# Performance work log

Hardware: AMD Instinct MI355X
Metric: run time of the kernel (lower is better)

## Reference

```python
import jax, jax.numpy as jnp
import numpy as np
from jax import lax

NPOINT = 1024   # FPS centroids
NSAMPLE = 32    # neighbors per ball
RADIUS = 0.1    # ball-query radius (points live in unit cube)


def farthest_point_sample(pos, npoint):
    # pos: [B, N, 3] -> idx [B, npoint] int32
    B, N, _ = pos.shape

    def step(carry, _):
        min_d, far = carry                                   # [B,N], [B]
        centroid = jnp.take_along_axis(pos, far[:, None, None], axis=1)  # [B,1,3]
        d = jnp.sum((pos - centroid) ** 2, axis=-1)          # [B,N]
        min_d = jnp.minimum(min_d, d)
        nxt = jnp.argmax(min_d, axis=1).astype(jnp.int32)
        return (min_d, nxt), far

    init = (jnp.full((B, N), 1e10, pos.dtype), jnp.zeros((B,), jnp.int32))
    _, idx = lax.scan(step, init, None, length=npoint)
    return idx.T                                             # [B, npoint]


def ball_query(new_pos, pos, radius, k):
    # new_pos: [B,M,3], pos: [B,N,3] -> idx [B,M,k] int32
    d2 = (jnp.sum(new_pos ** 2, -1)[:, :, None]
          + jnp.sum(pos ** 2, -1)[:, None, :]
          - 2.0 * jnp.einsum('bmc,bnc->bmn', new_pos, pos))  # [B,M,N]
    neg = jnp.where(d2 <= radius * radius, -d2, -jnp.inf)
    vals, idx = lax.top_k(neg, k)                            # k nearest inside ball
    valid = vals > -jnp.inf
    idx = jnp.where(valid, idx, idx[..., :1])                # replicate first hit (centroid itself)
    return idx.astype(jnp.int32)


def setup_inputs() -> dict:
    key = jax.random.key(0)
    ks = jax.random.split(key, 6)
    B, N, C = 4, 16384, 1
    pos = jax.random.uniform(ks[0], (B, N, 3), dtype=jnp.float32)
    x = jax.random.normal(ks[1], (B, N, C), dtype=jnp.float32)
    c_in = 3 + C  # rel-xyz concat features
    W1 = jax.random.normal(ks[2], (c_in, 32), jnp.float32) * np.sqrt(2.0 / c_in)
    W2 = jax.random.normal(ks[3], (32, 32), jnp.float32) * np.sqrt(2.0 / 32)
    W3 = jax.random.normal(ks[4], (32, 32), jnp.float32) * np.sqrt(2.0 / 32)
    b1 = jnp.zeros((32,), jnp.float32)
    b2 = jnp.zeros((32,), jnp.float32)
    b3 = jnp.zeros((32,), jnp.float32)
    return {"pos": pos, "x": x, "W1": W1, "b1": b1, "W2": W2, "b2": b2, "W3": W3, "b3": b3}


def reference(pos, x, W1, b1, W2, b2, W3, b3):
    # PointNet++ set-abstraction: FPS -> ball query -> group -> shared MLP -> max-pool.
    fps_idx = farthest_point_sample(lax.stop_gradient(pos), NPOINT)       # [B,M]
    new_pos = jnp.take_along_axis(pos, fps_idx[..., None], axis=1)        # [B,M,3]
    idx = ball_query(lax.stop_gradient(new_pos), lax.stop_gradient(pos), RADIUS, NSAMPLE)  # [B,M,K]
    B, M, K = idx.shape
    flat = idx.reshape(B, M * K)
    gpos = jnp.take_along_axis(pos, flat[..., None], axis=1).reshape(B, M, K, 3)
    gx = jnp.take_along_axis(x, flat[..., None], axis=1).reshape(B, M, K, -1)
    rel = gpos - new_pos[:, :, None, :]                                   # local coords
    h = jnp.concatenate([rel, gx], axis=-1)                               # [B,M,K,4]
    h = jax.nn.relu(h @ W1 + b1)
    h = jax.nn.relu(h @ W2 + b2)
    h = jax.nn.relu(h @ W3 + b3)
    return jnp.max(h, axis=2)                                             # [B,M,32]
```

## Files before the change

### kernel.cpp

```cpp
#include <hip/hip_runtime.h>

#define NB 4
#define NPT 16384
#define NPOINT 1024
#define NSAMPLE 32

#define FPS_T 512
#define FPS_PPT (NPT / FPS_T)

#define BQ_WAVES 4
#define CAP 896

template <int CTRL>
__device__ __forceinline__ float dpp_max_step(float v) {
  const int s =
      __builtin_amdgcn_update_dpp(0, __float_as_int(v), CTRL, 0xf, 0xf, true);
  return fmaxf(v, __int_as_float(s));
}

#define REP32(M)                                                              \
  M(0) M(1) M(2) M(3) M(4) M(5) M(6) M(7) M(8) M(9) M(10) M(11) M(12) M(13)  \
  M(14) M(15) M(16) M(17) M(18) M(19) M(20) M(21) M(22) M(23) M(24) M(25)    \
  M(26) M(27) M(28) M(29) M(30) M(31)

__global__ __launch_bounds__(FPS_T, 2) void fps_kernel(
    const float* __restrict__ pos, float* __restrict__ new_pos) {
#pragma clang fp contract(off)
  const int b = blockIdx.x;
  const int tid = threadIdx.x;
  const int wid = tid >> 6;
  const int lane = tid & 63;
  const float* __restrict__ p = pos + (size_t)b * NPT * 3;

  __shared__ float2 sxy[NPT];
  __shared__ float clog[NPOINT * 3];
  __shared__ unsigned long long red[3];
  __shared__ float wzs[3][8];

#define DECLPT(i) float X##i, Y##i, Z##i, MD##i;
  REP32(DECLPT)

  {
    const float4* pf4 = (const float4*)(p + (size_t)tid * (FPS_PPT * 3));
#define LODQ(p0, p1, p2, p3, A, B, C)                                         \
  X##p0 = A.x; Y##p0 = A.y; Z##p0 = A.z;                                      \
  X##p1 = A.w; Y##p1 = B.x; Z##p1 = B.y;                                      \
  X##p2 = B.z; Y##p2 = B.w; Z##p2 = C.x;                                      \
  X##p3 = C.y; Y##p3 = C.z; Z##p3 = C.w;
    {
      const float4 A = pf4[0], B = pf4[1], C = pf4[2];
      LODQ(0, 1, 2, 3, A, B, C)
    }
    {
      const float4 A = pf4[3], B = pf4[4], C = pf4[5];
      LODQ(4, 5, 6, 7, A, B, C)
    }
    {
      const float4 A = pf4[6], B = pf4[7], C = pf4[8];
      LODQ(8, 9, 10, 11, A, B, C)
    }
    {
      const float4 A = pf4[9], B = pf4[10], C = pf4[11];
      LODQ(12, 13, 14, 15, A, B, C)
    }
    {
      const float4 A = pf4[12], B = pf4[13], C = pf4[14];
      LODQ(16, 17, 18, 19, A, B, C)
    }
    {
      const float4 A = pf4[15], B = pf4[16], C = pf4[17];
      LODQ(20, 21, 22, 23, A, B, C)
    }
    {
      const float4 A = pf4[18], B = pf4[19], C = pf4[20];
      LODQ(24, 25, 26, 27, A, B, C)
    }
    {
      const float4 A = pf4[21], B = pf4[22], C = pf4[23];
      LODQ(28, 29, 30, 31, A, B, C)
    }
  }
#define INITMD(i) MD##i = 1e10f;
  REP32(INITMD)
#define STASHXY(i) sxy[(i)*FPS_T + tid] = make_float2(X##i, Y##i);
  REP32(STASHXY)

  if (tid < 3) red[tid] = 0ull;
  __syncthreads();

  float cx = p[0], cy = p[1], cz = p[2];

  for (int j = 0; j < NPOINT; ++j) {
    if (tid == 0) {
      clog[3 * j + 0] = cx;
      clog[3 * j + 1] = cy;
      clog[3 * j + 2] = cz;
    }
    float bm = -1.0f;
    int bi = 0;
    float bz = 0.0f;
#define SCAN(i)                                                               \
  {                                                                           \
    const float dx = X##i - cx;                                               \
    const float dy = Y##i - cy;                                               \
    const float dz = Z##i - cz;                                               \
    const float d = (dx * dx + dy * dy) + dz * dz;                            \
    const float m = fminf(MD##i, d);                                          \
    MD##i = m;                                                                \
    if (m > bm) {                                                             \
      bm = m;                                                                 \
      bi = i;                                                                 \
      bz = Z##i;                                                              \
    }                                                                         \
  }
    REP32(SCAN)
    float v = bm;
    v = dpp_max_step<0x111>(v);
    v = dpp_max_step<0x112>(v);
    v = dpp_max_step<0x114>(v);
    v = dpp_max_step<0x118>(v);
    v = dpp_max_step<0x142>(v);
    v = dpp_max_step<0x143>(v);
    const float wm =
        __int_as_float(__builtin_amdgcn_readlane(__float_as_int(v), 63));
    const unsigned long long tied = __ballot(bm == wm);
    const int wl = __ffsll((long long)tied) - 1;
    const int wbi = __builtin_amdgcn_readlane(bi, wl);
    const float wbz =
        __int_as_float(__builtin_amdgcn_readlane(__float_as_int(bz), wl));
    const int widx = ((wid << 6) + wl) * FPS_PPT + wbi;
    if (lane == 0) {
      const unsigned long long key =
          ((unsigned long long)__float_as_uint(wm) << 32) |
          (unsigned)(~widx);
      atomicMax(&red[j % 3], key);
      wzs[j % 3][wid] = wbz;
    }
    __syncthreads();
    const unsigned long long w = red[j % 3];
    if (tid == 0) red[(j + 2) % 3] = 0ull;
    const int nf = (int)(~(unsigned)w);
    cz = wzs[j % 3][nf >> 11];
    const int ot = nf >> 5;
    const int oi = nf & 31;
    const float2 cxy = sxy[oi * FPS_T + ot];
    cx = cxy.x;
    cy = cxy.y;
  }

  __syncthreads();
  for (int k = tid; k < NPOINT * 3; k += FPS_T)
    new_pos[(size_t)b * NPOINT * 3 + k] = clog[k];
}

__global__ __launch_bounds__(256) void bq_mlp_kernel(
    const float* __restrict__ pos, const float* __restrict__ x,
    const float* __restrict__ W1, const float* __restrict__ b1,
    const float* __restrict__ W2, const float* __restrict__ b2,
    const float* __restrict__ W3, const float* __restrict__ b3,
    const float* __restrict__ new_pos, float* __restrict__ out) {
#pragma clang fp contract(off)
  __shared__ __align__(16) float w1s[4 * 32];
  __shared__ __align__(16) float w2s[32 * 32];
  __shared__ __align__(16) float w3s[32 * 32];
  __shared__ float b1s[32], b2s[32], b3s[32];
  __shared__ unsigned long long list[BQ_WAVES][CAP];
  __shared__ int sel[BQ_WAVES][NSAMPLE];
  __shared__ unsigned cnt[BQ_WAVES];

  const int tid = threadIdx.x;
  const int wid = tid >> 6;
  const int lane = tid & 63;

  for (int i = tid; i < 128; i += 256) w1s[i] = W1[i];
  for (int i = tid; i < 1024; i += 256) {
    w2s[i] = W2[i];
    w3s[i] = W3[i];
  }
  if (tid < 32) {
    b1s[tid] = b1[tid];
    b2s[tid] = b2[tid];
    b3s[tid] = b3[tid];
  }
  if (lane == 0) cnt[wid] = 0u;
  __syncthreads();

  const int m_global = blockIdx.x * BQ_WAVES + wid;
  const int b = m_global >> 10;
  const float* __restrict__ p = pos + (size_t)b * NPT * 3;
  const float* __restrict__ xb = x + (size_t)b * NPT;

  const float cx = new_pos[(size_t)m_global * 3 + 0];
  const float cy = new_pos[(size_t)m_global * 3 + 1];
  const float cz = new_pos[(size_t)m_global * 3 + 2];
  const float snew = (cx * cx + cy * cy) + cz * cz;

  for (int it = 0; it < NPT / 256; ++it) {
    const int n0 = it * 256 + lane * 4;
    const float4* pf4 = (const float4*)(p + (size_t)n0 * 3);
    const float4 a = pf4[0];
    const float4 bq = pf4[1];
    const float4 c = pf4[2];
    float qx[4], qy[4], qz[4];
    qx[0] = a.x;  qy[0] = a.y;  qz[0] = a.z;
    qx[1] = a.w;  qy[1] = bq.x; qz[1] = bq.y;
    qx[2] = bq.z; qy[2] = bq.w; qz[2] = c.x;
    qx[3] = c.y;  qy[3] = c.z;  qz[3] = c.w;
#pragma unroll
    for (int t = 0; t < 4; ++t) {
      const float spos = (qx[t] * qx[t] + qy[t] * qy[t]) + qz[t] * qz[t];
      const float dot = (cx * qx[t] + cy * qy[t]) + cz * qz[t];
      const float d2 = (snew + spos) - 2.0f * dot;
      if (d2 <= 0.01f) {
        const unsigned u = __float_as_uint(d2);
        const unsigned key = (u & 0x80000000u) ? ~u : (u | 0x80000000u);
        const unsigned li = atomicAdd(&cnt[wid], 1u);
        if (li < CAP)
          list[wid][li] = ((unsigned long long)key << 32) | (unsigned)(n0 + t);
      }
    }
  }
  __syncthreads();

  int c = (int)cnt[wid];
  if (c > CAP) c = CAP;
  const int nsel = c < NSAMPLE ? c : NSAMPLE;

  for (int i = lane; i < c; i += 64) {
    const unsigned long long ki = list[wid][i];
    int rank = 0;
    for (int jj = 0; jj < c; ++jj) rank += (list[wid][jj] < ki) ? 1 : 0;
    if (rank < NSAMPLE) sel[wid][rank] = (int)(unsigned)(ki & 0xFFFFFFFFull);
  }
  __syncthreads();

  const bool active = (lane < nsel);
  const int n = sel[wid][active ? lane : 0];

  const float gpx = p[n * 3 + 0];
  const float gpy = p[n * 3 + 1];
  const float gpz = p[n * 3 + 2];
  const float gxv = xb[n];

  const float h0 = gpx - cx, h1i = gpy - cy, h2i = gpz - cz, h3i = gxv;

  float h1[32];
#pragma unroll
  for (int o = 0; o < 32; ++o) {
    float a = b1s[o];
    a += h0 * w1s[0 * 32 + o];
    a += h1i * w1s[1 * 32 + o];
    a += h2i * w1s[2 * 32 + o];
    a += h3i * w1s[3 * 32 + o];
    h1[o] = fmaxf(a, 0.0f);
  }

  float acc[32];
#pragma unroll
  for (int o = 0; o < 32; ++o) acc[o] = b2s[o];
  for (int k = 0; k < 32; ++k) {
    const float hk = h1[k];
    const float4* row = (const float4*)&w2s[k * 32];
#pragma unroll
    for (int q = 0; q < 8; ++q) {
      const float4 ww = row[q];
      acc[4 * q + 0] += hk * ww.x;
      acc[4 * q + 1] += hk * ww.y;
      acc[4 * q + 2] += hk * ww.z;
      acc[4 * q + 3] += hk * ww.w;
    }
  }
#pragma unroll
  for (int o = 0; o < 32; ++o) h1[o] = fmaxf(acc[o], 0.0f);

#pragma unroll
  for (int o = 0; o < 32; ++o) acc[o] = b3s[o];
  for (int k = 0; k < 32; ++k) {
    const float hk = h1[k];
    const float4* row = (const float4*)&w3s[k * 32];
#pragma unroll
    for (int q = 0; q < 8; ++q) {
      const float4 ww = row[q];
      acc[4 * q + 0] += hk * ww.x;
      acc[4 * q + 1] += hk * ww.y;
      acc[4 * q + 2] += hk * ww.z;
      acc[4 * q + 3] += hk * ww.w;
    }
  }
#pragma unroll
  for (int o = 0; o < 32; ++o)
    acc[o] = active ? fmaxf(acc[o], 0.0f) : -INFINITY;

#pragma unroll
  for (int mask = 1; mask <= 16; mask <<= 1) {
#pragma unroll
    for (int o = 0; o < 32; ++o)
      acc[o] = fmaxf(acc[o], __shfl_xor(acc[o], mask, 64));
  }

  if (lane == 0) {
    float4* o4 = (float4*)(out + (size_t)m_global * 32);
#pragma unroll
    for (int q = 0; q < 8; ++q)
      o4[q] = make_float4(acc[4 * q + 0], acc[4 * q + 1], acc[4 * q + 2],
                          acc[4 * q + 3]);
  }
}

extern "C" void kernel_launch(void* const* d_in, const int* in_sizes, int n_in,
                              void* d_out, int out_size, void* d_ws,
                              size_t ws_size, hipStream_t stream) {
  const float* pos = (const float*)d_in[0];
  const float* x = (const float*)d_in[1];
  const float* W1 = (const float*)d_in[2];
  const float* b1 = (const float*)d_in[3];
  const float* W2 = (const float*)d_in[4];
  const float* b2 = (const float*)d_in[5];
  const float* W3 = (const float*)d_in[6];
  const float* b3 = (const float*)d_in[7];
  float* out = (float*)d_out;
  float* new_pos = (float*)d_ws;

  fps_kernel<<<NB, FPS_T, 0, stream>>>(pos, new_pos);
  bq_mlp_kernel<<<(NB * NPOINT) / BQ_WAVES, 256, 0, stream>>>(
      pos, x, W1, b1, W2, b2, W3, b3, new_pos, out);
}
```

Measured before the change: 1.914 ms.

## Halve FPS block to 256 threads with 64 register-resident points each

Farthest point sampling now runs with 256 threads, each holding 64 points in registers, where before it used 512 threads holding 32. The winning wave's x, y and z are read out with readlane and published through small shared arrays, so the shared xy stash and its lookup go away. This cuts the block-wide barrier and atomic reduction to 4 waves per iteration. The cost is a longer serial per-thread scan and much higher register pressure (256 point values plus the pinning asm), with a risk of spilling.

```diff
diff --git a/kernel.cpp b/kernel.cpp
--- a/kernel.cpp
+++ b/kernel.cpp
@@ -5,25 +5,35 @@
 #define NPOINT 1024
 #define NSAMPLE 32
 
-#define FPS_T 512
-#define FPS_PPT (NPT / FPS_T)
+#define FPS_T 256
+#define FPS_PPT 64
 
 #define BQ_WAVES 4
 #define CAP 896
 
 template <int CTRL>
-__device__ __forceinline__ float dpp_max_step(float v) {
+__device__ __forceinline__ float dpp_fmax(float v) {
   const int s =
       __builtin_amdgcn_update_dpp(0, __float_as_int(v), CTRL, 0xf, 0xf, true);
   return fmaxf(v, __int_as_float(s));
 }
-
-#define REP32(M)                                                              \
+#define DPP_MAX_CHAIN(v)                                                      \
+  v = dpp_fmax<0x111>(v);                                                     \
+  v = dpp_fmax<0x112>(v);                                                     \
+  v = dpp_fmax<0x114>(v);                                                     \
+  v = dpp_fmax<0x118>(v);                                                     \
+  v = dpp_fmax<0x142>(v);                                                     \
+  v = dpp_fmax<0x143>(v);
+
+#define REP64(M)                                                              \
   M(0) M(1) M(2) M(3) M(4) M(5) M(6) M(7) M(8) M(9) M(10) M(11) M(12) M(13)  \
   M(14) M(15) M(16) M(17) M(18) M(19) M(20) M(21) M(22) M(23) M(24) M(25)    \
-  M(26) M(27) M(28) M(29) M(30) M(31)
-
-__global__ __launch_bounds__(FPS_T, 2) void fps_kernel(
+  M(26) M(27) M(28) M(29) M(30) M(31) M(32) M(33) M(34) M(35) M(36) M(37)    \
+  M(38) M(39) M(40) M(41) M(42) M(43) M(44) M(45) M(46) M(47) M(48) M(49)    \
+  M(50) M(51) M(52) M(53) M(54) M(55) M(56) M(57) M(58) M(59) M(60) M(61)    \
+  M(62) M(63)
+
+__global__ __launch_bounds__(FPS_T, 1) void fps_kernel(
     const float* __restrict__ pos, float* __restrict__ new_pos) {
 #pragma clang fp contract(off)
   const int b = blockIdx.x;
@@ -32,58 +42,42 @@
   const int lane = tid & 63;
   const float* __restrict__ p = pos + (size_t)b * NPT * 3;
 
-  __shared__ float2 sxy[NPT];
   __shared__ float clog[NPOINT * 3];
   __shared__ unsigned long long red[3];
-  __shared__ float wzs[3][8];
+  __shared__ float wxs[3][4], wys[3][4], wzs[3][4];
 
 #define DECLPT(i) float X##i, Y##i, Z##i, MD##i;
-  REP32(DECLPT)
+  REP64(DECLPT)
 
   {
     const float4* pf4 = (const float4*)(p + (size_t)tid * (FPS_PPT * 3));
-#define LODQ(p0, p1, p2, p3, A, B, C)                                         \
-  X##p0 = A.x; Y##p0 = A.y; Z##p0 = A.z;                                      \
-  X##p1 = A.w; Y##p1 = B.x; Z##p1 = B.y;                                      \
-  X##p2 = B.z; Y##p2 = B.w; Z##p2 = C.x;                                      \
-  X##p3 = C.y; Y##p3 = C.z; Z##p3 = C.w;
-    {
-      const float4 A = pf4[0], B = pf4[1], C = pf4[2];
-      LODQ(0, 1, 2, 3, A, B, C)
-    }
-    {
-      const float4 A = pf4[3], B = pf4[4], C = pf4[5];
-      LODQ(4, 5, 6, 7, A, B, C)
-    }
-    {
-      const float4 A = pf4[6], B = pf4[7], C = pf4[8];
-      LODQ(8, 9, 10, 11, A, B, C)
-    }
-    {
-      const float4 A = pf4[9], B = pf4[10], C = pf4[11];
-      LODQ(12, 13, 14, 15, A, B, C)
-    }
-    {
-      const float4 A = pf4[12], B = pf4[13], C = pf4[14];
-      LODQ(16, 17, 18, 19, A, B, C)
-    }
-    {
-      const float4 A = pf4[15], B = pf4[16], C = pf4[17];
-      LODQ(20, 21, 22, 23, A, B, C)
-    }
-    {
-      const float4 A = pf4[18], B = pf4[19], C = pf4[20];
-      LODQ(24, 25, 26, 27, A, B, C)
-    }
-    {
-      const float4 A = pf4[21], B = pf4[22], C = pf4[23];
-      LODQ(28, 29, 30, 31, A, B, C)
-    }
+#define LODG(g, p0, p1, p2, p3)                                               \
+  {                                                                           \
+    const float4 A = pf4[3 * (g)], B = pf4[3 * (g) + 1], C = pf4[3 * (g) + 2];\
+    X##p0 = A.x; Y##p0 = A.y; Z##p0 = A.z;                                    \
+    X##p1 = A.w; Y##p1 = B.x; Z##p1 = B.y;                                    \
+    X##p2 = B.z; Y##p2 = B.w; Z##p2 = C.x;                                    \
+    X##p3 = C.y; Y##p3 = C.z; Z##p3 = C.w;                                    \
+  }
+    LODG(0, 0, 1, 2, 3)
+    LODG(1, 4, 5, 6, 7)
+    LODG(2, 8, 9, 10, 11)
+    LODG(3, 12, 13, 14, 15)
+    LODG(4, 16, 17, 18, 19)
+    LODG(5, 20, 21, 22, 23)
+    LODG(6, 24, 25, 26, 27)
+    LODG(7, 28, 29, 30, 31)
+    LODG(8, 32, 33, 34, 35)
+    LODG(9, 36, 37, 38, 39)
+    LODG(10, 40, 41, 42, 43)
+    LODG(11, 44, 45, 46, 47)
+    LODG(12, 48, 49, 50, 51)
+    LODG(13, 52, 53, 54, 55)
+    LODG(14, 56, 57, 58, 59)
+    LODG(15, 60, 61, 62, 63)
   }
 #define INITMD(i) MD##i = 1e10f;
-  REP32(INITMD)
-#define STASHXY(i) sxy[(i)*FPS_T + tid] = make_float2(X##i, Y##i);
-  REP32(STASHXY)
+  REP64(INITMD)
 
   if (tid < 3) red[tid] = 0ull;
   __syncthreads();
@@ -91,6 +85,9 @@
   float cx = p[0], cy = p[1], cz = p[2];
 
   for (int j = 0; j < NPOINT; ++j) {
+#define PIN3(i) asm volatile("" : "+v"(X##i), "+v"(Y##i), "+v"(Z##i));
+    REP64(PIN3)
+
     if (tid == 0) {
       clog[3 * j + 0] = cx;
       clog[3 * j + 1] = cy;
@@ -98,7 +95,7 @@
     }
     float bm = -1.0f;
     int bi = 0;
-    float bz = 0.0f;
+    float bx = 0.0f, by = 0.0f, bz = 0.0f;
 #define SCAN(i)                                                               \
   {                                                                           \
     const float dx = X##i - cx;                                               \
@@ -110,22 +107,23 @@
     if (m > bm) {                                                             \
       bm = m;                                                                 \
       bi = i;                                                                 \
+      bx = X##i;                                                              \
+      by = Y##i;                                                              \
       bz = Z##i;                                                              \
     }                                                                         \
   }
-    REP32(SCAN)
+    REP64(SCAN)
     float v = bm;
-    v = dpp_max_step<0x111>(v);
-    v = dpp_max_step<0x112>(v);
-    v = dpp_max_step<0x114>(v);
-    v = dpp_max_step<0x118>(v);
-    v = dpp_max_step<0x142>(v);
-    v = dpp_max_step<0x143>(v);
+    DPP_MAX_CHAIN(v)
     const float wm =
         __int_as_float(__builtin_amdgcn_readlane(__float_as_int(v), 63));
     const unsigned long long tied = __ballot(bm == wm);
     const int wl = __ffsll((long long)tied) - 1;
     const int wbi = __builtin_amdgcn_readlane(bi, wl);
+    const float wbx =
+        __int_as_float(__builtin_amdgcn_readlane(__float_as_int(bx), wl));
+    const float wby =
+        __int_as_float(__builtin_amdgcn_readlane(__float_as_int(by), wl));
     const float wbz =
         __int_as_float(__builtin_amdgcn_readlane(__float_as_int(bz), wl));
     const int widx = ((wid << 6) + wl) * FPS_PPT + wbi;
@@ -134,18 +132,18 @@
           ((unsigned long long)__float_as_uint(wm) << 32) |
           (unsigned)(~widx);
       atomicMax(&red[j % 3], key);
+      wxs[j % 3][wid] = wbx;
+      wys[j % 3][wid] = wby;
       wzs[j % 3][wid] = wbz;
     }
     __syncthreads();
     const unsigned long long w = red[j % 3];
     if (tid == 0) red[(j + 2) % 3] = 0ull;
-    const int nf = (int)(~(unsigned)w);
-    cz = wzs[j % 3][nf >> 11];
-    const int ot = nf >> 5;
-    const int oi = nf & 31;
-    const float2 cxy = sxy[oi * FPS_T + ot];
-    cx = cxy.x;
-    cy = cxy.y;
+    const unsigned nf = ~(unsigned)w;
+    const int wv = (int)(nf >> 12);
+    cx = wxs[j % 3][wv];
+    cy = wys[j % 3][wv];
+    cz = wzs[j % 3][wv];
   }
 
   __syncthreads();
```

After: 3.052 ms. +59.4%, slower.
